# Kernel tuning notes

Measured on AMD Instinct MI355X. Metric: run time of the kernel, lower is better.

## Reference

```python
import jax, jax.numpy as jnp
import numpy as np

B, S, R = 8, 4096, 512
E, K, ATOMS, XAR, TOPK = 64, 256, 16, 3, 2
TEMP = 1.0


def setup_inputs() -> dict:
    key = jax.random.key(0)
    k0, k1, k2, k3, k4 = jax.random.split(key, 5)
    x_latent = jax.random.normal(k0, (B, S, R), jnp.float32)
    router_w = jax.random.normal(k1, (E, R), jnp.float32) * (1.0 / np.sqrt(R))
    atoms = jax.random.normal(k2, (E, ATOMS, R), jnp.float32) * 0.01
    combo_weights = jax.random.uniform(k3, (E, K, XAR), jnp.float32) * 0.5 + 0.25
    combo_logits = jax.random.normal(k4, (E, K, XAR, ATOMS), jnp.float32) * 0.01
    return {"x_latent": x_latent, "router_w": router_w, "atoms": atoms,
            "combo_weights": combo_weights, "combo_logits": combo_logits}


def _expert_centroids(atoms, combo_weights, combo_logits):
    # Hard codeword path (vectorized over experts):
    # sign atoms -> pick argmax atom per (k, xor slot) -> weight -> sum -> sign -> mean over k
    binary = jnp.sign(atoms)                                   # [E, A, R]
    # softmax(logits/t) then argmax == argmax(logits) (monotone)
    idx = jnp.argmax(combo_logits, axis=-1)                    # [E, K, XAR]
    sel = binary[jnp.arange(E)[:, None, None], idx]            # [E, K, XAR, R]
    codewords = jnp.sign((sel * combo_weights[..., None]).sum(axis=2))  # [E, K, R]
    return codewords.mean(axis=1)                              # [E, R]


def reference(x_latent, router_w, atoms, combo_weights, combo_logits):
    t = max(TEMP, 0.1)
    router_logits = jnp.einsum('bsr,er->bse', x_latent, router_w)   # [B, S, E]
    probs_t = jax.nn.softmax(router_logits / t, axis=-1)
    gates, expert_ids = jax.lax.top_k(probs_t, TOPK)                # [B, S, 2]
    gates = gates / gates.sum(axis=-1, keepdims=True)

    centroids = _expert_centroids(atoms, combo_weights, combo_logits)  # [E, R]

    # aux load-balancing loss (uses untempered softmax)
    router_prob = jax.nn.softmax(router_logits, axis=-1)
    aux_loss = E * jnp.sum(router_prob.mean(axis=(0, 1)) *
                           (router_prob > 0).astype(x_latent.dtype).mean(axis=(0, 1)))

    # dense per-expert gate = sum over topk slots of gate * (id == e), then combine with centroids
    dense_gates = (jax.nn.one_hot(expert_ids, E, dtype=gates.dtype) *
                   gates[..., None]).sum(axis=-2)                    # [B, S, E]
    combined = jnp.einsum('bse,er->bsr', dense_gates, centroids)     # [B, S, R]
    return combined, aux_loss
```

## Files before the change

### kernel.cpp

```cpp
#include <hip/hip_runtime.h>
#include <math.h>

#define TOKENS 32768
#define RDIM 512
#define NEXP 64
#define NK 256
#define LDK 136
#define TAU 4.0e-3f

typedef unsigned short u16;
typedef float f32x4 __attribute__((ext_vector_type(4)));
typedef short s16x8 __attribute__((ext_vector_type(8)));

#define MFMA_B16(a, b, c) __builtin_amdgcn_mfma_f32_16x16x32_bf16(a, b, c, 0, 0, 0)

__device__ __forceinline__ void split_pack(float4 v, unsigned& h01, unsigned& h23,
                                           unsigned& l01, unsigned& l23) {
    unsigned u0 = __float_as_uint(v.x), u1 = __float_as_uint(v.y);
    unsigned u2 = __float_as_uint(v.z), u3 = __float_as_uint(v.w);
    float r0 = v.x - __uint_as_float(u0 & 0xFFFF0000u);
    float r1 = v.y - __uint_as_float(u1 & 0xFFFF0000u);
    float r2 = v.z - __uint_as_float(u2 & 0xFFFF0000u);
    float r3 = v.w - __uint_as_float(u3 & 0xFFFF0000u);
    h01 = (u0 >> 16) | (u1 & 0xFFFF0000u);
    h23 = (u2 >> 16) | (u3 & 0xFFFF0000u);
    l01 = (__float_as_uint(r0) >> 16) | (__float_as_uint(r1) & 0xFFFF0000u);
    l23 = (__float_as_uint(r2) >> 16) | (__float_as_uint(r3) & 0xFFFF0000u);
}

__global__ __launch_bounds__(256) void centroid_kernel(
    const float* __restrict__ atoms,
    const float* __restrict__ cw,
    const float* __restrict__ cl,
    float* __restrict__ cent,
    float* __restrict__ aux_sum,
    unsigned* __restrict__ aux_cnt)
{
    __shared__ unsigned pack[NK];
    const int e    = blockIdx.x >> 1;
    const int half = blockIdx.x & 1;
    const int tid  = threadIdx.x;

    if (blockIdx.x == 0 && tid < 64) { aux_sum[tid] = 0.f; aux_cnt[tid] = 0u; }

    {
        const int k = tid;
        unsigned u = 0;
        float w3[3];
        #pragma unroll
        for (int xx = 0; xx < 3; ++xx) {
            const float* cp = cl + ((((size_t)e * NK + k) * 3 + xx) << 4);
            float v[16];
            *(float4*)(v + 0)  = *(const float4*)(cp + 0);
            *(float4*)(v + 4)  = *(const float4*)(cp + 4);
            *(float4*)(v + 8)  = *(const float4*)(cp + 8);
            *(float4*)(v + 12) = *(const float4*)(cp + 12);
            float best = v[0]; int bi = 0;
            #pragma unroll
            for (int a = 1; a < 16; ++a) {
                if (v[a] > best) { best = v[a]; bi = a; }
            }
            u |= (unsigned)bi << (4 * xx);
            w3[xx] = cw[((size_t)e * NK + k) * 3 + xx];
        }
        unsigned lut = 0;
        #pragma unroll
        for (int c = 0; c < 8; ++c) {
            float val = ((c & 1) ? -w3[0] : w3[0])
                      + ((c & 2) ? -w3[1] : w3[1])
                      + ((c & 4) ? -w3[2] : w3[2]);
            lut |= (val < 0.f ? 1u : 0u) << c;
        }
        pack[k] = u | (lut << 16);
    }

    const int r = half * 256 + tid;
    unsigned B0 = 0;
    #pragma unroll
    for (int a = 0; a < 16; ++a)
        B0 |= (atoms[((size_t)e * 16 + a) * RDIM + r] < 0.f ? 1u : 0u) << a;
    __syncthreads();

    int n0 = 0;
    for (int k = 0; k < NK; ++k) {
        unsigned u  = pack[k];
        unsigned i0 = u & 15u, i1 = (u >> 4) & 15u, i2 = (u >> 8) & 15u;
        unsigned c0 = ((B0 >> i0) & 1u) | (((B0 >> i1) & 1u) << 1) | (((B0 >> i2) & 1u) << 2);
        n0 += (u >> (16 + c0)) & 1u;
    }
    cent[(size_t)e * RDIM + r] = 1.f - (float)n0 * (1.f / 128.f);
}

__global__ __launch_bounds__(256) void moe_main(
    const float* __restrict__ x,
    const float* __restrict__ w,
    const float* __restrict__ cent,
    float* __restrict__ out,
    float* __restrict__ aux_sum,
    unsigned* __restrict__ aux_cnt)
{
    __shared__ f32x4 smem4[4352];
    u16* xhi = (u16*)smem4;
    u16* xlo = xhi + 64 * LDK;
    u16* whi = xhi + 2 * 64 * LDK;
    u16* wlo = xhi + 3 * 64 * LDK;
    float* P = (float*)smem4;
    __shared__ float s_aux[64];
    __shared__ unsigned s_cnt[64];

    const int tid  = threadIdx.x;
    const int lane = tid & 63;
    const int wave = tid >> 6;
    const int tok0 = blockIdx.x * 64;
    const int l15  = lane & 15;
    const int kgrp = (lane >> 4) << 3;

    if (tid < 64) { s_aux[tid] = 0.f; s_cnt[tid] = 0u; }

    f32x4 acc[4];
    #pragma unroll
    for (int nt = 0; nt < 4; ++nt) acc[nt] = (f32x4){0.f, 0.f, 0.f, 0.f};

    const int kq4  = (tid & 31) << 2;
    const int row0 = tid >> 5;
    const float* xg = x + (size_t)(tok0 + row0) * RDIM + kq4;
    const float* wg = w + (size_t)row0 * RDIM + kq4;
    const int ldsoff = row0 * LDK + kq4;

    float4 xr[8], wr[8];
    #pragma unroll
    for (int j = 0; j < 8; ++j) {
        xr[j] = *(const float4*)(xg + (size_t)j * 8 * RDIM);
        wr[j] = *(const float4*)(wg + (size_t)j * 8 * RDIM);
    }

    const int arow = (wave << 4) + l15;

    for (int c = 0; c < 4; ++c) {
        __syncthreads();
        #pragma unroll
        for (int j = 0; j < 8; ++j) {
            unsigned h01, h23, l01, l23;
            split_pack(xr[j], h01, h23, l01, l23);
            *(uint2*)&xhi[ldsoff + j * 8 * LDK] = make_uint2(h01, h23);
            *(uint2*)&xlo[ldsoff + j * 8 * LDK] = make_uint2(l01, l23);
            split_pack(wr[j], h01, h23, l01, l23);
            *(uint2*)&whi[ldsoff + j * 8 * LDK] = make_uint2(h01, h23);
            *(uint2*)&wlo[ldsoff + j * 8 * LDK] = make_uint2(l01, l23);
        }
        __syncthreads();
        if (c < 3) {
            const int o = (c + 1) * 128;
            #pragma unroll
            for (int j = 0; j < 8; ++j) {
                xr[j] = *(const float4*)(xg + o + (size_t)j * 8 * RDIM);
                wr[j] = *(const float4*)(wg + o + (size_t)j * 8 * RDIM);
            }
        }
        #pragma unroll
        for (int s = 0; s < 4; ++s) {
            const int kb = s * 32 + kgrp;
            s16x8 ah = *(const s16x8*)&xhi[arow * LDK + kb];
            s16x8 al = *(const s16x8*)&xlo[arow * LDK + kb];
            #pragma unroll
            for (int nt = 0; nt < 4; ++nt) {
                const int brow = (nt << 4) + l15;
                s16x8 bh = *(const s16x8*)&whi[brow * LDK + kb];
                s16x8 bl = *(const s16x8*)&wlo[brow * LDK + kb];
                acc[nt] = MFMA_B16(ah, bh, acc[nt]);
                acc[nt] = MFMA_B16(ah, bl, acc[nt]);
                acc[nt] = MFMA_B16(al, bh, acc[nt]);
            }
        }
    }

    __syncthreads();
    #pragma unroll
    for (int nt = 0; nt < 4; ++nt)
        #pragma unroll
        for (int i = 0; i < 4; ++i)
            P[((wave << 4) + ((lane >> 4) << 2) + i) * 66 + nt * 16 + l15] = acc[nt][i];
    __syncthreads();

    float regsum = 0.f;
    int   regcnt = 0;
    const int e = lane;
    for (int s2 = 0; s2 < 16; ++s2) {
        const int tt = (wave << 4) + s2;
        const float val = P[tt * 66 + e];

        float m1 = val; int i1 = e;
        #pragma unroll
        for (int off = 32; off; off >>= 1) {
            float ov = __shfl_xor(m1, off);
            int   oi = __shfl_xor(i1, off);
            if (ov > m1 || (ov == m1 && oi < i1)) { m1 = ov; i1 = oi; }
        }
        float m2 = (e == i1) ? -INFINITY : val; int i2 = e;
        #pragma unroll
        for (int off = 32; off; off >>= 1) {
            float ov = __shfl_xor(m2, off);
            int   oi = __shfl_xor(i2, off);
            if (ov > m2 || (ov == m2 && oi < i2)) { m2 = ov; i2 = oi; }
        }
        float m3 = (e == i1 || e == i2) ? -INFINITY : val; int i3 = e;
        #pragma unroll
        for (int off = 32; off; off >>= 1) {
            float ov = __shfl_xor(m3, off);
            int   oi = __shfl_xor(i3, off);
            if (ov > m3 || (ov == m3 && oi < i3)) { m3 = ov; i3 = oi; }
        }

        float g1v = m1, g2v = m2; int e1 = i1, e2 = i2;
        if (m2 - m3 < TAU) {
            const float* xrow = x + (size_t)(tok0 + tt) * RDIM + e * 8;
            float4 a0 = *(const float4*)(xrow);
            float4 a1 = *(const float4*)(xrow + 4);
            float d[3]; int id3[3] = { i1, i2, i3 };
            #pragma unroll
            for (int j = 0; j < 3; ++j) {
                const float* wrow = w + (size_t)id3[j] * RDIM + e * 8;
                float4 b0 = *(const float4*)(wrow);
                float4 b1 = *(const float4*)(wrow + 4);
                float p = a0.x * b0.x;
                p = fmaf(a0.y, b0.y, p); p = fmaf(a0.z, b0.z, p); p = fmaf(a0.w, b0.w, p);
                p = fmaf(a1.x, b1.x, p); p = fmaf(a1.y, b1.y, p);
                p = fmaf(a1.z, b1.z, p); p = fmaf(a1.w, b1.w, p);
                #pragma unroll
                for (int off = 32; off; off >>= 1) p += __shfl_xor(p, off);
                d[j] = p;
            }
            int b = 0;
            if (d[1] > d[0] || (d[1] == d[0] && id3[1] < id3[0])) b = 1;
            if (d[2] > d[b] || (d[2] == d[b] && id3[2] < id3[b])) b = 2;
            int sec;
            if (b == 0)      sec = (d[1] > d[2] || (d[1] == d[2] && id3[1] < id3[2])) ? 1 : 2;
            else if (b == 1) sec = (d[0] > d[2] || (d[0] == d[2] && id3[0] < id3[2])) ? 0 : 2;
            else             sec = (d[0] > d[1] || (d[0] == d[1] && id3[0] < id3[1])) ? 0 : 1;
            g1v = d[b];   e1 = id3[b];
            g2v = d[sec]; e2 = id3[sec];
        }

        const float ex = expf(val - m1);
        float Z = ex;
        #pragma unroll
        for (int off = 32; off; off >>= 1) Z += __shfl_xor(Z, off);
        regsum += ex / Z;
        regcnt += (ex > 0.f) ? 1 : 0;

        const float ed  = expf(g2v - g1v);
        const float inv = 1.f / (1.f + ed);
        const float g1 = inv, g2 = ed * inv;

        const float4* c1 = (const float4*)(cent + (size_t)e1 * RDIM);
        const float4* c2 = (const float4*)(cent + (size_t)e2 * RDIM);
        float4* op = (float4*)(out + (size_t)(tok0 + tt) * RDIM);
        float4 A0 = c1[e],      Bb0 = c2[e];
        float4 A1 = c1[e + 64], Bb1 = c2[e + 64];
        float4 o0, o1;
        o0.x = fmaf(g1, A0.x, g2 * Bb0.x); o0.y = fmaf(g1, A0.y, g2 * Bb0.y);
        o0.z = fmaf(g1, A0.z, g2 * Bb0.z); o0.w = fmaf(g1, A0.w, g2 * Bb0.w);
        o1.x = fmaf(g1, A1.x, g2 * Bb1.x); o1.y = fmaf(g1, A1.y, g2 * Bb1.y);
        o1.z = fmaf(g1, A1.z, g2 * Bb1.z); o1.w = fmaf(g1, A1.w, g2 * Bb1.w);
        op[e]      = o0;
        op[e + 64] = o1;
    }

    atomicAdd(&s_aux[e], regsum);
    atomicAdd(&s_cnt[e], (unsigned)regcnt);
    __syncthreads();
    if (tid < 64) {
        atomicAdd(aux_sum + tid, s_aux[tid]);
        atomicAdd(aux_cnt + tid, s_cnt[tid]);
    }
}

__global__ __launch_bounds__(64) void aux_kernel(
    const float* __restrict__ sums,
    const unsigned* __restrict__ cnts,
    float* __restrict__ out_aux)
{
    const int e = threadIdx.x;
    float v = (sums[e] * (1.f / (float)TOKENS)) * ((float)cnts[e] * (1.f / (float)TOKENS));
    #pragma unroll
    for (int off = 32; off; off >>= 1) v += __shfl_xor(v, off);
    if (e == 0) out_aux[0] = (float)NEXP * v;
}

extern "C" void kernel_launch(void* const* d_in, const int* in_sizes, int n_in,
                              void* d_out, int out_size, void* d_ws, size_t ws_size,
                              hipStream_t stream) {
    const float* x     = (const float*)d_in[0];
    const float* rw    = (const float*)d_in[1];
    const float* atoms = (const float*)d_in[2];
    const float* cwts  = (const float*)d_in[3];
    const float* clog  = (const float*)d_in[4];
    float* out = (float*)d_out;

    float*    aux_sum = (float*)d_ws;
    unsigned* aux_cnt = (unsigned*)((char*)d_ws + 256);
    float*    cent    = (float*)((char*)d_ws + 512);

    centroid_kernel<<<128, 256, 0, stream>>>(atoms, cwts, clog, cent, aux_sum, aux_cnt);
    moe_main<<<512, 256, 0, stream>>>(x, rw, cent, out, aux_sum, aux_cnt);
    aux_kernel<<<1, 64, 0, stream>>>(aux_sum, aux_cnt, out + (size_t)TOKENS * RDIM);
}
```

Baseline: 172.5 us.

## Double block threads and parallelize top-k/softmax epilogue across waves per token

```diff
diff --git a/kernel.cpp b/kernel.cpp
--- a/kernel.cpp
+++ b/kernel.cpp
@@ -6,6 +6,7 @@
 #define NEXP 64
 #define NK 256
 #define LDK 136
+#define PSTR 67
 #define TAU 4.0e-3f
 
 typedef unsigned short u16;
@@ -91,7 +92,7 @@
     cent[(size_t)e * RDIM + r] = 1.f - (float)n0 * (1.f / 128.f);
 }
 
-__global__ __launch_bounds__(256) void moe_main(
+__global__ __launch_bounds__(512, 4) void moe_main(
     const float* __restrict__ x,
     const float* __restrict__ w,
     const float* __restrict__ cent,
@@ -104,22 +105,28 @@
     u16* xlo = xhi + 64 * LDK;
     u16* whi = xhi + 2 * 64 * LDK;
     u16* wlo = xhi + 3 * 64 * LDK;
-    float* P = (float*)smem4;
+    float* P     = (float*)smem4;
+    float* candv = P + 64 * PSTR;
+    int*   candi = (int*)(candv + 64 * 25);
+    float* qsum  = (float*)(candi + 64 * 25);
+    float* gateL = qsum + 64 * 9;
     __shared__ float s_aux[64];
     __shared__ unsigned s_cnt[64];
 
     const int tid  = threadIdx.x;
     const int lane = tid & 63;
     const int wave = tid >> 6;
-    const int tok0 = blockIdx.x * 64;
     const int l15  = lane & 15;
     const int kgrp = (lane >> 4) << 3;
+    const int tok0 = blockIdx.x * 64;
+    const int tokG = wave >> 1;
+    const int expG = wave & 1;
 
     if (tid < 64) { s_aux[tid] = 0.f; s_cnt[tid] = 0u; }
 
-    f32x4 acc[4];
-    #pragma unroll
-    for (int nt = 0; nt < 4; ++nt) acc[nt] = (f32x4){0.f, 0.f, 0.f, 0.f};
+    f32x4 acc[2];
+    acc[0] = (f32x4){0.f,0.f,0.f,0.f};
+    acc[1] = (f32x4){0.f,0.f,0.f,0.f};
 
     const int kq4  = (tid & 31) << 2;
     const int row0 = tid >> 5;
@@ -127,34 +134,34 @@
     const float* wg = w + (size_t)row0 * RDIM + kq4;
     const int ldsoff = row0 * LDK + kq4;
 
-    float4 xr[8], wr[8];
-    #pragma unroll
-    for (int j = 0; j < 8; ++j) {
-        xr[j] = *(const float4*)(xg + (size_t)j * 8 * RDIM);
-        wr[j] = *(const float4*)(wg + (size_t)j * 8 * RDIM);
-    }
-
-    const int arow = (wave << 4) + l15;
+    uint2 xh2[4], xl2[4], wh2[4], wl2[4];
+    #pragma unroll
+    for (int j = 0; j < 4; ++j) {
+        float4 a = *(const float4*)(xg + (size_t)j * 16 * RDIM);
+        float4 b = *(const float4*)(wg + (size_t)j * 16 * RDIM);
+        split_pack(a, xh2[j].x, xh2[j].y, xl2[j].x, xl2[j].y);
+        split_pack(b, wh2[j].x, wh2[j].y, wl2[j].x, wl2[j].y);
+    }
+
+    const int arow = tokG * 16 + l15;
 
     for (int c = 0; c < 4; ++c) {
         __syncthreads();
         #pragma unroll
-        for (int j = 0; j < 8; ++j) {
-            unsigned h01, h23, l01, l23;
-            split_pack(xr[j], h01, h23, l01, l23);
-            *(uint2*)&xhi[ldsoff + j * 8 * LDK] = make_uint2(h01, h23);
-            *(uint2*)&xlo[ldsoff + j * 8 * LDK] = make_uint2(l01, l23);
-            split_pack(wr[j], h01, h23, l01, l23);
-            *(uint2*)&whi[ldsoff + j * 8 * LDK] = make_uint2(h01, h23);
-            *(uint2*)&wlo[ldsoff + j * 8 * LDK] = make_uint2(l01, l23);
+        for (int j = 0; j < 4; ++j) {
+            *(uint2*)&xhi[ldsoff + j * 16 * LDK] = xh2[j];
+            *(uint2*)&xlo[ldsoff + j * 16 * LDK] = xl2[j];
+            *(uint2*)&whi[ldsoff + j * 16 * LDK] = wh2[j];
+            *(uint2*)&wlo[ldsoff + j * 16 * LDK] = wl2[j];
         }
         __syncthreads();
+        float4 fa[4], fb[4];
         if (c < 3) {
             const int o = (c + 1) * 128;
             #pragma unroll
-            for (int j = 0; j < 8; ++j) {
-                xr[j] = *(const float4*)(xg + o + (size_t)j * 8 * RDIM);
-                wr[j] = *(const float4*)(wg + o + (size_t)j * 8 * RDIM);
+            for (int j = 0; j < 4; ++j) {
+                fa[j] = *(const float4*)(xg + o + (size_t)j * 16 * RDIM);
+                fb[j] = *(const float4*)(wg + o + (size_t)j * 16 * RDIM);
             }
         }
         #pragma unroll
@@ -163,8 +170,8 @@
             s16x8 ah = *(const s16x8*)&xhi[arow * LDK + kb];
             s16x8 al = *(const s16x8*)&xlo[arow * LDK + kb];
             #pragma unroll
-            for (int nt = 0; nt < 4; ++nt) {
-                const int brow = (nt << 4) + l15;
+            for (int nt = 0; nt < 2; ++nt) {
+                const int brow = expG * 32 + nt * 16 + l15;
                 s16x8 bh = *(const s16x8*)&whi[brow * LDK + kb];
                 s16x8 bl = *(const s16x8*)&wlo[brow * LDK + kb];
                 acc[nt] = MFMA_B16(ah, bh, acc[nt]);
@@ -172,63 +179,73 @@
                 acc[nt] = MFMA_B16(al, bh, acc[nt]);
             }
         }
-    }
-
-    __syncthreads();
-    #pragma unroll
-    for (int nt = 0; nt < 4; ++nt)
+        if (c < 3) {
+            #pragma unroll
+            for (int j = 0; j < 4; ++j) {
+                split_pack(fa[j], xh2[j].x, xh2[j].y, xl2[j].x, xl2[j].y);
+                split_pack(fb[j], wh2[j].x, wh2[j].y, wl2[j].x, wl2[j].y);
+            }
+        }
+    }
+
+    __syncthreads();
+    #pragma unroll
+    for (int nt = 0; nt < 2; ++nt)
         #pragma unroll
         for (int i = 0; i < 4; ++i)
-            P[((wave << 4) + ((lane >> 4) << 2) + i) * 66 + nt * 16 + l15] = acc[nt][i];
-    __syncthreads();
-
-    float regsum = 0.f;
-    int   regcnt = 0;
-    const int e = lane;
-    for (int s2 = 0; s2 < 16; ++s2) {
-        const int tt = (wave << 4) + s2;
-        const float val = P[tt * 66 + e];
-
-        float m1 = val; int i1 = e;
-        #pragma unroll
-        for (int off = 32; off; off >>= 1) {
-            float ov = __shfl_xor(m1, off);
-            int   oi = __shfl_xor(i1, off);
-            if (ov > m1 || (ov == m1 && oi < i1)) { m1 = ov; i1 = oi; }
-        }
-        float m2 = (e == i1) ? -INFINITY : val; int i2 = e;
-        #pragma unroll
-        for (int off = 32; off; off >>= 1) {
-            float ov = __shfl_xor(m2, off);
-            int   oi = __shfl_xor(i2, off);
-            if (ov > m2 || (ov == m2 && oi < i2)) { m2 = ov; i2 = oi; }
-        }
-        float m3 = (e == i1 || e == i2) ? -INFINITY : val; int i3 = e;
-        #pragma unroll
-        for (int off = 32; off; off >>= 1) {
-            float ov = __shfl_xor(m3, off);
-            int   oi = __shfl_xor(i3, off);
-            if (ov > m3 || (ov == m3 && oi < i3)) { m3 = ov; i3 = oi; }
-        }
-
+            P[(tokG * 16 + ((lane >> 4) << 2) + i) * PSTR + expG * 32 + nt * 16 + l15] = acc[nt][i];
+    __syncthreads();
+
+    const int tt = tid & 63;
+    const int ss = tid >> 6;
+    float v[8];
+    #pragma unroll
+    for (int j = 0; j < 8; ++j) v[j] = P[tt * PSTR + ss * 8 + j];
+
+    float m1 = -INFINITY, m2 = -INFINITY, m3 = -INFINITY;
+    int   i1 = NEXP, i2 = NEXP, i3 = NEXP;
+    #pragma unroll
+    for (int j = 0; j < 8; ++j) {
+        float val = v[j]; int e = ss * 8 + j;
+        if (val > m1)      { m3 = m2; i3 = i2; m2 = m1; i2 = i1; m1 = val; i1 = e; }
+        else if (val > m2) { m3 = m2; i3 = i2; m2 = val; i2 = e; }
+        else if (val > m3) { m3 = val; i3 = e; }
+    }
+    candv[tt * 25 + ss * 3 + 0] = m1; candi[tt * 25 + ss * 3 + 0] = i1;
+    candv[tt * 25 + ss * 3 + 1] = m2; candi[tt * 25 + ss * 3 + 1] = i2;
+    candv[tt * 25 + ss * 3 + 2] = m3; candi[tt * 25 + ss * 3 + 2] = i3;
+    __syncthreads();
+
+    m1 = m2 = m3 = -INFINITY; i1 = i2 = i3 = NEXP;
+    #pragma unroll
+    for (int q = 0; q < 24; ++q) {
+        float val = candv[tt * 25 + q]; int e = candi[tt * 25 + q];
+        if (val > m1)      { m3 = m2; i3 = i2; m2 = m1; i2 = i1; m1 = val; i1 = e; }
+        else if (val > m2) { m3 = m2; i3 = i2; m2 = val; i2 = e; }
+        else if (val > m3) { m3 = val; i3 = e; }
+    }
+
+    float ex[8]; float ps = 0.f;
+    #pragma unroll
+    for (int j = 0; j < 8; ++j) { ex[j] = __expf(v[j] - m1); ps += ex[j]; }
+    qsum[tt * 9 + ss] = ps;
+
+    if (ss == 0) {
         float g1v = m1, g2v = m2; int e1 = i1, e2 = i2;
         if (m2 - m3 < TAU) {
-            const float* xrow = x + (size_t)(tok0 + tt) * RDIM + e * 8;
-            float4 a0 = *(const float4*)(xrow);
-            float4 a1 = *(const float4*)(xrow + 4);
+            const float* xrow = x + (size_t)(tok0 + tt) * RDIM;
             float d[3]; int id3[3] = { i1, i2, i3 };
-            #pragma unroll
-            for (int j = 0; j < 3; ++j) {
-                const float* wrow = w + (size_t)id3[j] * RDIM + e * 8;
-                float4 b0 = *(const float4*)(wrow);
-                float4 b1 = *(const float4*)(wrow + 4);
-                float p = a0.x * b0.x;
-                p = fmaf(a0.y, b0.y, p); p = fmaf(a0.z, b0.z, p); p = fmaf(a0.w, b0.w, p);
-                p = fmaf(a1.x, b1.x, p); p = fmaf(a1.y, b1.y, p);
-                p = fmaf(a1.z, b1.z, p); p = fmaf(a1.w, b1.w, p);
-                #pragma unroll
-                for (int off = 32; off; off >>= 1) p += __shfl_xor(p, off);
-                d[j] = p;
+            for (int jj = 0; jj < 3; ++jj) {
+                const float* wrow = w + (size_t)id3[jj] * RDIM;
+                float p = 0.f;
+                #pragma unroll 4
+                for (int k = 0; k < RDIM; k += 4) {
+                    float4 a = *(const float4*)(xrow + k);
+                    float4 b = *(const float4*)(wrow + k);
+                    p = fmaf(a.x, b.x, p); p = fmaf(a.y, b.y, p);
+                    p = fmaf(a.z, b.z, p); p = fmaf(a.w, b.w, p);
+                }
+                d[jj] = p;
             }
             int b = 0;
             if (d[1] > d[0] || (d[1] == d[0] && id3[1] < id3[0])) b = 1;
@@ -240,38 +257,61 @@
             g1v = d[b];   e1 = id3[b];
             g2v = d[sec]; e2 = id3[sec];
         }
-
-        const float ex = expf(val - m1);
-        float Z = ex;
-        #pragma unroll
-        for (int off = 32; off; off >>= 1) Z += __shfl_xor(Z, off);
-        regsum += ex / Z;
-        regcnt += (ex > 0.f) ? 1 : 0;
-
-        const float ed  = expf(g2v - g1v);
+        const float ed  = __expf(g2v - g1v);
         const float inv = 1.f / (1.f + ed);
-        const float g1 = inv, g2 = ed * inv;
-
-        const float4* c1 = (const float4*)(cent + (size_t)e1 * RDIM);
-        const float4* c2 = (const float4*)(cent + (size_t)e2 * RDIM);
-        float4* op = (float4*)(out + (size_t)(tok0 + tt) * RDIM);
-        float4 A0 = c1[e],      Bb0 = c2[e];
-        float4 A1 = c1[e + 64], Bb1 = c2[e + 64];
-        float4 o0, o1;
-        o0.x = fmaf(g1, A0.x, g2 * Bb0.x); o0.y = fmaf(g1, A0.y, g2 * Bb0.y);
-        o0.z = fmaf(g1, A0.z, g2 * Bb0.z); o0.w = fmaf(g1, A0.w, g2 * Bb0.w);
-        o1.x = fmaf(g1, A1.x, g2 * Bb1.x); o1.y = fmaf(g1, A1.y, g2 * Bb1.y);
-        o1.z = fmaf(g1, A1.z, g2 * Bb1.z); o1.w = fmaf(g1, A1.w, g2 * Bb1.w);
-        op[e]      = o0;
-        op[e + 64] = o1;
-    }
-
-    atomicAdd(&s_aux[e], regsum);
-    atomicAdd(&s_cnt[e], (unsigned)regcnt);
+        gateL[tt * 4 + 0] = inv;
+        gateL[tt * 4 + 1] = ed * inv;
+        ((int*)gateL)[tt * 4 + 2] = e1;
+        ((int*)gateL)[tt * 4 + 3] = e2;
+    }
+    __syncthreads();
+
+    float Z = 0.f;
+    #pragma unroll
+    for (int k = 0; k < 8; ++k) Z += qsum[tt * 9 + k];
+    const float invZ = 1.f / Z;
+    #pragma unroll
+    for (int j = 0; j < 8; ++j) P[tt * PSTR + ss * 8 + j] = ex[j] * invZ;
+    __syncthreads();
+
+    {
+        const int e = tid & 63, tq = tid >> 6;
+        float s = 0.f; unsigned cn = 0u;
+        #pragma unroll
+        for (int t = 0; t < 8; ++t) {
+            float pv = P[(tq * 8 + t) * PSTR + e];
+            s += pv; cn += (pv > 0.f) ? 1u : 0u;
+        }
+        atomicAdd(&s_aux[e], s);
+        atomicAdd(&s_cnt[e], cn);
+    }
     __syncthreads();
     if (tid < 64) {
         atomicAdd(aux_sum + tid, s_aux[tid]);
         atomicAdd(aux_cnt + tid, s_cnt[tid]);
+    }
+
+    {
+        const int e = lane;
+        #pragma unroll
+        for (int s2 = 0; s2 < 8; ++s2) {
+            const int t2 = wave * 8 + s2;
+            float4 g4 = *(float4*)&gateL[t2 * 4];
+            const float g1 = g4.x, g2 = g4.y;
+            const int e1 = __float_as_int(g4.z), e2 = __float_as_int(g4.w);
+            const float4* c1 = (const float4*)(cent + (size_t)e1 * RDIM);
+            const float4* c2 = (const float4*)(cent + (size_t)e2 * RDIM);
+            float4* op = (float4*)(out + (size_t)(tok0 + t2) * RDIM);
+            float4 A0 = c1[e],      Bb0 = c2[e];
+            float4 A1 = c1[e + 64], Bb1 = c2[e + 64];
+            float4 o0, o1;
+            o0.x = fmaf(g1, A0.x, g2 * Bb0.x); o0.y = fmaf(g1, A0.y, g2 * Bb0.y);
+            o0.z = fmaf(g1, A0.z, g2 * Bb0.z); o0.w = fmaf(g1, A0.w, g2 * Bb0.w);
+            o1.x = fmaf(g1, A1.x, g2 * Bb1.x); o1.y = fmaf(g1, A1.y, g2 * Bb1.y);
+            o1.z = fmaf(g1, A1.z, g2 * Bb1.z); o1.w = fmaf(g1, A1.w, g2 * Bb1.w);
+            op[e]      = o0;
+            op[e + 64] = o1;
+        }
     }
 }
 
@@ -302,6 +342,6 @@
     float*    cent    = (float*)((char*)d_ws + 512);
 
     centroid_kernel<<<128, 256, 0, stream>>>(atoms, cwts, clog, cent, aux_sum, aux_cnt);
-    moe_main<<<512, 256, 0, stream>>>(x, rw, cent, out, aux_sum, aux_cnt);
+    moe_main<<<512, 512, 0, stream>>>(x, rw, cent, out, aux_sum, aux_cnt);
     aux_kernel<<<1, 64, 0, stream>>>(aux_sum, aux_cnt, out + (size_t)TOKENS * RDIM);
 }
```

Measured after the change: 163.5 us. 1.06x faster.
